# Kernel tuning notes

Measured on AMD Instinct MI355X. Metric: run time of the kernel, lower is better.

The kernel has to match this reference:

```python
import jax, jax.numpy as jnp
import numpy as np
import math

NUM_HEADS = 12


def setup_inputs() -> dict:
    key = jax.random.key(0)
    ks = jax.random.split(key, 8)
    B, H, W, C = 8, 32, 32, 768
    dh = C // NUM_HEADS
    s = 0.02
    return {
        "x": jax.random.normal(ks[0], (B, H, W, C), dtype=jnp.float32),
        "w_qkv": jax.random.normal(ks[1], (C, 3 * C), dtype=jnp.float32) * s,
        "b_qkv": jnp.zeros((3 * C,), dtype=jnp.float32),
        "w_out": jax.random.normal(ks[2], (C, C), dtype=jnp.float32) * s,
        "b_out": jnp.zeros((C,), dtype=jnp.float32),
        "rel_pos_h": jax.random.normal(ks[3], (2 * H - 1, dh), dtype=jnp.float32) * s,
        "rel_pos_w": jax.random.normal(ks[4], (2 * W - 1, dh), dtype=jnp.float32) * s,
    }


def reference(x, w_qkv, b_qkv, w_out, b_out, rel_pos_h, rel_pos_w):
    B, H, W, C = x.shape
    nh = NUM_HEADS
    dh = C // nh
    scale = math.sqrt(dh)

    # QKV projection: (B, H*W, 3C) -> (3, B*nh, H*W, dh)
    qkv = jnp.einsum("bhwc,cf->bhwf", x, w_qkv) + b_qkv
    qkv = qkv.reshape(B, H * W, 3, nh, dh).transpose(2, 0, 3, 1, 4)
    qkv = qkv.reshape(3, B * nh, H * W, dh)
    q, k, v = qkv[0], qkv[1], qkv[2]

    scores = jnp.einsum("bqd,bkd->bqk", q, k) / scale  # (B*nh, HW, HW)

    # Decomposed relative position bias (q_size == k_size == input_size,
    # so get_rel_pos is a pure gather, no interpolation).
    coords_h = jnp.arange(H)[:, None] - jnp.arange(H)[None, :] + (H - 1)
    coords_w = jnp.arange(W)[:, None] - jnp.arange(W)[None, :] + (W - 1)
    Rh = rel_pos_h[coords_h]  # (H, H, dh)
    Rw = rel_pos_w[coords_w]  # (W, W, dh)
    r_q = q.reshape(B * nh, H, W, dh)
    rel_h = jnp.einsum("bhwc,hkc->bhwk", r_q, Rh)  # (B*nh, H, W, H)
    rel_w = jnp.einsum("bhwc,wkc->bhwk", r_q, Rw)  # (B*nh, H, W, W)
    scores = (
        scores.reshape(B * nh, H, W, H, W)
        + rel_h[:, :, :, :, None]
        + rel_w[:, :, :, None, :]
    ).reshape(B * nh, H * W, H * W)

    weights = jax.nn.softmax(scores, axis=-1)
    out = jnp.einsum("bqk,bkd->bqd", weights, v)  # (B*nh, HW, dh)
    out = out.reshape(B, nh, H, W, dh).transpose(0, 2, 3, 1, 4).reshape(B, H, W, C)
    return jnp.einsum("bhwc,cf->bhwf", out, w_out) + b_out
```

## Files before the change

kernel.cpp:

```cpp
#include <hip/hip_runtime.h>
#include <stdint.h>

#define NH 12
#define DH 64
#define HW_ 32
#define SEQ 1024
#define CDIM 768
#define BATCH 8
#define BHN (BATCH*NH)

#define LOG2E 1.44269504f
#define KSCALE 0.18033688f

typedef unsigned short u16;
typedef __attribute__((ext_vector_type(4))) float f32x4;
typedef __attribute__((ext_vector_type(8))) short bf16x8;

static __device__ __forceinline__ u16 f2bf(float f) {
  union { float f; unsigned u; } v; v.f = f;
  unsigned r = v.u + 0x7fff + ((v.u >> 16) & 1);
  return (u16)(r >> 16);
}
static __device__ __forceinline__ float bf2f(u16 h) {
  union { unsigned u; float f; } v; v.u = ((unsigned)h) << 16;
  return v.f;
}
static __device__ __forceinline__ unsigned pk_bf2(float a, float b) {
  union { float f; unsigned u; } ua, ub; ua.f = a; ub.f = b;
  return __builtin_amdgcn_perm(ub.u + 0x8000u, ua.u + 0x8000u, 0x07060302u);
}

#define GLDS(gp, lp) __builtin_amdgcn_global_load_lds( \
  (const __attribute__((address_space(1))) unsigned int*)(gp), \
  (__attribute__((address_space(3))) unsigned int*)(lp), 16, 0, 0)

__global__ void k_cvt_x(const float* __restrict__ x, u16* __restrict__ xb, int n4) {
  int i = blockIdx.x * 256 + threadIdx.x;
  if (i < n4) {
    const float4 v = *(const float4*)(x + (size_t)i * 4);
    uint2 o;
    o.x = (unsigned)f2bf(v.x) | ((unsigned)f2bf(v.y) << 16);
    o.y = (unsigned)f2bf(v.z) | ((unsigned)f2bf(v.w) << 16);
    *(uint2*)(xb + (size_t)i * 4) = o;
  }
}

__global__ void k_transcvt(const float* __restrict__ w, u16* __restrict__ wt, int R, int C) {
  __shared__ float t[64][65];
  int c0 = blockIdx.x * 64, r0 = blockIdx.y * 64;
  #pragma unroll
  for (int i = 0; i < 16; ++i) {
    int r = threadIdx.y + i * 4;
    t[r][threadIdx.x] = w[(size_t)(r0 + r) * C + c0 + threadIdx.x];
  }
  __syncthreads();
  #pragma unroll
  for (int i = 0; i < 16; ++i) {
    int c = threadIdx.y + i * 4;
    wt[(size_t)(c0 + c) * R + r0 + threadIdx.x] = f2bf(t[threadIdx.x][c]);
  }
}

__global__ __launch_bounds__(256) void k_relbias2(
    const u16* __restrict__ Q, const float* __restrict__ rph,
    const float* __restrict__ rpw,
    float* __restrict__ bH, float* __restrict__ bW) {
  __shared__ float Gs[4][64][66];
  const int bh = blockIdx.y;
  const int tid = threadIdx.x, w = tid >> 6, l = tid & 63;
  const int rr = l & 15, g4 = l >> 4;
  const int p0 = blockIdx.x * 256 + w * 64;
  const u16* Qb = Q + ((size_t)bh * SEQ + p0) * DH;

  bf16x8 qa[4][2];
  #pragma unroll
  for (int rt = 0; rt < 4; ++rt)
    #pragma unroll
    for (int kk = 0; kk < 2; ++kk)
      qa[rt][kk] = *(const bf16x8*)&Qb[(size_t)(rt * 16 + rr) * DH + kk * 32 + g4 * 8];

  const int hq0 = p0 >> 5;
  #pragma unroll
  for (int g = 0; g < 2; ++g) {
    int hq = hq0 + g;
    #pragma unroll
    for (int ct = 0; ct < 2; ++ct) {
      bf16x8 bfr[2];
      #pragma unroll
      for (int kk = 0; kk < 2; ++kk) {
        const float* src = &rph[(size_t)(hq - (ct * 16 + rr) + 31) * DH + kk * 32 + g4 * 8];
        #pragma unroll
        for (int e = 0; e < 8; ++e) bfr[kk][e] = (short)f2bf(src[e]);
      }
      #pragma unroll
      for (int mt = 0; mt < 2; ++mt) {
        f32x4 acc = {};
        #pragma unroll
        for (int kk = 0; kk < 2; ++kk)
          acc = __builtin_amdgcn_mfma_f32_16x16x32_bf16(qa[g * 2 + mt][kk], bfr[kk], acc, 0, 0, 0);
        #pragma unroll
        for (int j = 0; j < 4; ++j) {
          int row = p0 + g * 32 + mt * 16 + g4 * 4 + j;
          bH[((size_t)bh * SEQ + row) * 32 + ct * 16 + rr] = acc[j] * LOG2E;
        }
      }
    }
  }

  #pragma unroll
  for (int jt = 0; jt < 4; ++jt) {
    int j_ = jt * 16 + rr; if (j_ > 62) j_ = 62;
    bf16x8 bfr[2];
    #pragma unroll
    for (int kk = 0; kk < 2; ++kk) {
      const float* src = &rpw[(size_t)j_ * DH + kk * 32 + g4 * 8];
      #pragma unroll
      for (int e = 0; e < 8; ++e) bfr[kk][e] = (short)f2bf(src[e]);
    }
    #pragma unroll
    for (int rt = 0; rt < 4; ++rt) {
      f32x4 acc = {};
      #pragma unroll
      for (int kk = 0; kk < 2; ++kk)
        acc = __builtin_amdgcn_mfma_f32_16x16x32_bf16(qa[rt][kk], bfr[kk], acc, 0, 0, 0);
      #pragma unroll
      for (int j = 0; j < 4; ++j)
        Gs[w][rt * 16 + g4 * 4 + j][jt * 16 + rr] = acc[j] * LOG2E;
    }
  }
  __syncthreads();
  #pragma unroll
  for (int wk = 0; wk < 32; ++wk)
    bW[((size_t)bh * SEQ + p0 + l) * 32 + wk] = Gs[w][l][(l & 31) - wk + 31];
}

template<int EPI, int NT>
__global__ __launch_bounds__(256) void k_gemm(
    const u16* __restrict__ A, const u16* __restrict__ Bt,
    const float* __restrict__ bias,
    void* __restrict__ o0, void* __restrict__ o1, void* __restrict__ o2,
    int nwg) {
  __shared__ u16 As[2][128][32];
  __shared__ u16 Bs[2][128][32];
  const int cpx = nwg >> 3;
  const int swz = (blockIdx.x & 7) * cpx + (blockIdx.x >> 3);
  const int tid = threadIdx.x, w = tid >> 6, l = tid & 63;
  const int wr = w >> 1, wc = w & 1;
  const int rr = l & 15, g4 = l >> 4;
  const int m0 = (swz / NT) * 128, n0 = (swz % NT) * 128;
  const int K = CDIM;
  f32x4 acc[4][4] = {};

  auto stage = [&](int buf, int t) {
    int k0 = t * 32;
    #pragma unroll
    for (int i = 0; i < 2; ++i) {
      int c = tid + i * 256;
      int row = c >> 2, kc = (c & 3) * 8;
      GLDS(A + (size_t)(m0 + row) * K + k0 + kc, ((u16*)As) + buf * 4096 + c * 8);
      GLDS(Bt + (size_t)(n0 + row) * K + k0 + kc, ((u16*)Bs) + buf * 4096 + c * 8);
    }
  };
  stage(0, 0);
  __syncthreads();
  for (int t = 0; t < K / 32; ++t) {
    const int cur = t & 1;
    if (t + 1 < K / 32) stage(cur ^ 1, t + 1);
    bf16x8 af[4], bfr[4];
    #pragma unroll
    for (int mm = 0; mm < 4; ++mm)
      af[mm] = *(const bf16x8*)(((const u16*)As) + cur * 4096 + (wr * 64 + mm * 16 + rr) * 32 + g4 * 8);
    #pragma unroll
    for (int nn = 0; nn < 4; ++nn)
      bfr[nn] = *(const bf16x8*)(((const u16*)Bs) + cur * 4096 + (wc * 64 + nn * 16 + rr) * 32 + g4 * 8);
    __builtin_amdgcn_s_setprio(1);
    #pragma unroll
    for (int mm = 0; mm < 4; ++mm)
      #pragma unroll
      for (int nn = 0; nn < 4; ++nn)
        acc[mm][nn] = __builtin_amdgcn_mfma_f32_16x16x32_bf16(af[mm], bfr[nn], acc[mm][nn], 0, 0, 0);
    __builtin_amdgcn_s_setprio(0);
    __syncthreads();
  }
  #pragma unroll
  for (int mm = 0; mm < 4; ++mm)
    #pragma unroll
    for (int nn = 0; nn < 4; ++nn) {
      int row0 = m0 + wr * 64 + mm * 16 + g4 * 4;
      int col = n0 + wc * 64 + nn * 16 + rr;
      float bb = bias[col];
      if (EPI == 0) {
        int which = col / CDIM, rem = col % CDIM;
        int hh = rem >> 6, d = rem & 63;
        int b = row0 >> 10, p = row0 & 1023;
        if (which == 2) {
          uint2 pk;
          pk.x = (unsigned)f2bf(acc[mm][nn][0] + bb) | ((unsigned)f2bf(acc[mm][nn][1] + bb) << 16);
          pk.y = (unsigned)f2bf(acc[mm][nn][2] + bb) | ((unsigned)f2bf(acc[mm][nn][3] + bb) << 16);
          *(uint2*)&((u16*)o2)[((size_t)(b * NH + hh) * DH + d) * SEQ + p] = pk;
        } else if (which == 1) {
          #pragma unroll
          for (int j = 0; j < 4; ++j)
            ((u16*)o1)[(((size_t)(b * NH + hh)) * SEQ + p + j) * DH + d] = f2bf((acc[mm][nn][j] + bb) * KSCALE);
        } else {
          #pragma unroll
          for (int j = 0; j < 4; ++j)
            ((u16*)o0)[(((size_t)(b * NH + hh)) * SEQ + p + j) * DH + d] = f2bf(acc[mm][nn][j] + bb);
        }
      } else {
        #pragma unroll
        for (int j = 0; j < 4; ++j)
          ((float*)o0)[(size_t)(row0 + j) * CDIM + col] = acc[mm][nn][j] + bb;
      }
    }
}

__global__ __launch_bounds__(256) void k_attn(
    const u16* __restrict__ Q, const u16* __restrict__ Kg,
    const u16* __restrict__ Vtg,
    const float* __restrict__ bHg, const float* __restrict__ bWg,
    u16* __restrict__ O) {
  __shared__ u16 Ks[2][64][64];
  __shared__ u16 Vs[2][64][64];
  __shared__ u16 Ps[4][32][72];
  const int bid = blockIdx.x;
  const int bhi = bid % 96;
  const int q0 = (bid / 96) * 128;
  const int tid = threadIdx.x, w = tid >> 6, l = tid & 63;
  const int rr = l & 15, g4 = l >> 4;
  const u16* Qb = Q + (size_t)bhi * SEQ * DH;
  const u16* Kb = Kg + (size_t)bhi * SEQ * DH;
  const u16* Vb = Vtg + (size_t)bhi * SEQ * DH;

  bf16x8 qf[2][2];
  #pragma unroll
  for (int mm = 0; mm < 2; ++mm)
    #pragma unroll
    for (int kk = 0; kk < 2; ++kk)
      qf[mm][kk] = *(const bf16x8*)&Qb[(size_t)(q0 + w * 32 + mm * 16 + rr) * DH + kk * 32 + g4 * 8];

  int ibase[2][4];
  float4 bwv[2][4];
  #pragma unroll
  for (int mm = 0; mm < 2; ++mm)
    #pragma unroll
    for (int j = 0; j < 4; ++j) {
      int p_e = q0 + w * 32 + mm * 16 + g4 * 4 + j;
      ibase[mm][j] = (bhi * SEQ + p_e) * 32;
      bwv[mm][j] = *(const float4*)&bWg[ibase[mm][j] + ((4 * rr) & 31)];
    }
  float lsum[2][4] = {};
  f32x4 oacc[2][4] = {};

  auto stageKV = [&](int buf, int t) {
    int k0 = t * 64;
    #pragma unroll
    for (int i = 0; i < 2; ++i) {
      int c = tid + i * 256;
      int row = c >> 3, ci = c & 7;
      int swk = ci ^ ((row >> 2) & 7);
      int swv = ci ^ (row & 7);
      GLDS(Kb + (size_t)(k0 + row) * DH + swk * 8, ((u16*)Ks) + buf * 4096 + c * 8);
      GLDS(Vb + (size_t)row * SEQ + k0 + swv * 8, ((u16*)Vs) + buf * 4096 + c * 8);
    }
  };
  stageKV(0, 0);
  __syncthreads();

  for (int t = 0; t < 16; ++t) {
    const int cur = t & 1;
    if (t + 1 < 16) stageKV(cur ^ 1, t + 1);

    bf16x8 kf[4][2];
    #pragma unroll
    for (int nn = 0; nn < 4; ++nn)
      #pragma unroll
      for (int kk = 0; kk < 2; ++kk) {
        int row = 4 * rr + nn;
        int ch = (kk * 4 + g4) ^ ((row >> 2) & 7);
        kf[nn][kk] = *(const bf16x8*)(((const u16*)Ks) + cur * 4096 + row * 64 + ch * 8);
      }
    f32x4 sc[2][4] = {};
    __builtin_amdgcn_s_setprio(1);
    #pragma unroll
    for (int mm = 0; mm < 2; ++mm)
      #pragma unroll
      for (int nn = 0; nn < 4; ++nn)
        #pragma unroll
        for (int kk = 0; kk < 2; ++kk)
          sc[mm][nn] = __builtin_amdgcn_mfma_f32_16x16x32_bf16(qf[mm][kk], kf[nn][kk], sc[mm][nn], 0, 0, 0);
    __builtin_amdgcn_s_setprio(0);

    #pragma unroll
    for (int mm = 0; mm < 2; ++mm)
      #pragma unroll
      for (int j = 0; j < 4; ++j) {
        float bh = bHg[ibase[mm][j] + t * 2 + (rr >> 3)];
        float v0 = __builtin_amdgcn_exp2f(sc[mm][0][j] + (bh + bwv[mm][j].x));
        float v1 = __builtin_amdgcn_exp2f(sc[mm][1][j] + (bh + bwv[mm][j].y));
        float v2 = __builtin_amdgcn_exp2f(sc[mm][2][j] + (bh + bwv[mm][j].z));
        float v3 = __builtin_amdgcn_exp2f(sc[mm][3][j] + (bh + bwv[mm][j].w));
        lsum[mm][j] += (v0 + v1) + (v2 + v3);
        uint2 pk;
        pk.x = pk_bf2(v0, v1);
        pk.y = pk_bf2(v2, v3);
        int prow = mm * 16 + g4 * 4 + j;
        *(uint2*)&Ps[w][prow][4 * rr] = pk;
      }

    bf16x8 pa[2][2], vf[4][2];
    #pragma unroll
    for (int mm = 0; mm < 2; ++mm)
      #pragma unroll
      for (int kk = 0; kk < 2; ++kk)
        pa[mm][kk] = *(const bf16x8*)&Ps[w][mm * 16 + rr][kk * 32 + g4 * 8];
    #pragma unroll
    for (int nn = 0; nn < 4; ++nn)
      #pragma unroll
      for (int kk = 0; kk < 2; ++kk) {
        int row = nn * 16 + rr;
        int ch = (kk * 4 + g4) ^ (row & 7);
        vf[nn][kk] = *(const bf16x8*)(((const u16*)Vs) + cur * 4096 + row * 64 + ch * 8);
      }
    __builtin_amdgcn_s_setprio(1);
    #pragma unroll
    for (int mm = 0; mm < 2; ++mm)
      #pragma unroll
      for (int nn = 0; nn < 4; ++nn)
        #pragma unroll
        for (int kk = 0; kk < 2; ++kk)
          oacc[mm][nn] = __builtin_amdgcn_mfma_f32_16x16x32_bf16(pa[mm][kk], vf[nn][kk], oacc[mm][nn], 0, 0, 0);
    __builtin_amdgcn_s_setprio(0);
    __syncthreads();
  }

  const int b = bhi / NH, h = bhi % NH;
  #pragma unroll
  for (int mm = 0; mm < 2; ++mm)
    #pragma unroll
    for (int j = 0; j < 4; ++j) {
      float lv = lsum[mm][j];
      #pragma unroll
      for (int off = 1; off < 16; off <<= 1) lv += __shfl_xor(lv, off);
      float inv = 1.0f / lv;
      int p = q0 + w * 32 + mm * 16 + g4 * 4 + j;
      #pragma unroll
      for (int nn = 0; nn < 4; ++nn) {
        int d = nn * 16 + rr;
        O[((size_t)(b * SEQ + p)) * CDIM + h * DH + d] = f2bf(oacc[mm][nn][j] * inv);
      }
    }
}

extern "C" void kernel_launch(void* const* d_in, const int* in_sizes, int n_in,
                              void* d_out, int out_size, void* d_ws, size_t ws_size,
                              hipStream_t stream) {
  const float* x     = (const float*)d_in[0];
  const float* w_qkv = (const float*)d_in[1];
  const float* b_qkv = (const float*)d_in[2];
  const float* w_out = (const float*)d_in[3];
  const float* b_out = (const float*)d_in[4];
  const float* rph   = (const float*)d_in[5];
  const float* rpw   = (const float*)d_in[6];
  float* out = (float*)d_out;
  char* ws = (char*)d_ws;

  const size_t SZ = (size_t)BHN * SEQ * DH * 2;
  u16* Xb    = (u16*)(ws);
  u16* Wqkvt = (u16*)(ws + SZ);
  u16* Woutt = (u16*)(ws + SZ + 3538944);
  u16* Qd    = (u16*)(ws + SZ + 4718592);
  u16* Kd    = (u16*)(ws + 2 * SZ + 4718592);
  u16* Vd    = (u16*)(ws + 3 * SZ + 4718592);
  u16* Vt    = (u16*)(ws + 4 * SZ + 4718592);
  float* bW  = (float*)(ws + 5 * SZ + 4718592);
  float* bH  = (float*)Vd;
  u16* Ob    = Xb;
  if (ws_size < 6 * SZ + 4718592) return;

  k_cvt_x<<<6144, 256, 0, stream>>>(x, Xb, 8192 * 768 / 4);
  k_transcvt<<<dim3(36, 12), dim3(64, 4), 0, stream>>>(w_qkv, Wqkvt, 768, 2304);
  k_transcvt<<<dim3(12, 12), dim3(64, 4), 0, stream>>>(w_out, Woutt, 768, 768);
  k_gemm<0, 18><<<1152, 256, 0, stream>>>(Xb, Wqkvt, b_qkv, Qd, Kd, Vt, 1152);
  k_relbias2<<<dim3(4, 96), 256, 0, stream>>>(Qd, rph, rpw, bH, bW);
  k_attn<<<768, 256, 0, stream>>>(Qd, Kd, Vt, bH, bW, Ob);
  k_gemm<1, 6><<<384, 256, 0, stream>>>(Ob, Woutt, b_out, out, nullptr, nullptr, 384);
}
```

Measured before the change: 163.4 us.

## Split attention block across 8 waves of 16 query rows each

The attention kernel now launches 512 threads per block, so each wave owns 16 query rows instead of 32. This halves per-thread accumulator and fragment registers and doubles the waves sharing each staged K/V tile; each thread now issues one async load per tile instead of two. The per-tile height bias global load is replaced by preloading 32 bias values into two registers per row and fetching the needed one with a cross-lane shuffle. The trade-off is that each wave re-reads the full K/V fragments from LDS for half as much MFMA work, raising LDS traffic per FLOP, and the block barrier now spans more waves.

New measurement: 156.3 us. 1.04x faster.

```diff
diff --git a/kernel.cpp b/kernel.cpp
--- a/kernel.cpp
+++ b/kernel.cpp
@@ -215,14 +215,14 @@
     }
 }
 
-__global__ __launch_bounds__(256) void k_attn(
+__global__ __launch_bounds__(512, 4) void k_attn(
     const u16* __restrict__ Q, const u16* __restrict__ Kg,
     const u16* __restrict__ Vtg,
     const float* __restrict__ bHg, const float* __restrict__ bWg,
     u16* __restrict__ O) {
   __shared__ u16 Ks[2][64][64];
   __shared__ u16 Vs[2][64][64];
-  __shared__ u16 Ps[4][32][72];
+  __shared__ u16 Ps[8][16][72];
   const int bid = blockIdx.x;
   const int bhi = bid % 96;
   const int q0 = (bid / 96) * 128;
@@ -232,37 +232,33 @@
   const u16* Kb = Kg + (size_t)bhi * SEQ * DH;
   const u16* Vb = Vtg + (size_t)bhi * SEQ * DH;
 
-  bf16x8 qf[2][2];
-  #pragma unroll
-  for (int mm = 0; mm < 2; ++mm)
-    #pragma unroll
-    for (int kk = 0; kk < 2; ++kk)
-      qf[mm][kk] = *(const bf16x8*)&Qb[(size_t)(q0 + w * 32 + mm * 16 + rr) * DH + kk * 32 + g4 * 8];
-
-  int ibase[2][4];
-  float4 bwv[2][4];
-  #pragma unroll
-  for (int mm = 0; mm < 2; ++mm)
-    #pragma unroll
-    for (int j = 0; j < 4; ++j) {
-      int p_e = q0 + w * 32 + mm * 16 + g4 * 4 + j;
-      ibase[mm][j] = (bhi * SEQ + p_e) * 32;
-      bwv[mm][j] = *(const float4*)&bWg[ibase[mm][j] + ((4 * rr) & 31)];
-    }
-  float lsum[2][4] = {};
-  f32x4 oacc[2][4] = {};
+  bf16x8 qf[2];
+  #pragma unroll
+  for (int kk = 0; kk < 2; ++kk)
+    qf[kk] = *(const bf16x8*)&Qb[(size_t)(q0 + w * 16 + rr) * DH + kk * 32 + g4 * 8];
+
+  float4 bwv[4];
+  float bh0[4], bh1[4];
+  float lsum[4] = {};
+  f32x4 oacc[4] = {};
+  #pragma unroll
+  for (int j = 0; j < 4; ++j) {
+    int p_e = q0 + w * 16 + g4 * 4 + j;
+    const float* bHrow = &bHg[((size_t)bhi * SEQ + p_e) * 32];
+    const float* bWrow = &bWg[((size_t)bhi * SEQ + p_e) * 32];
+    bwv[j] = *(const float4*)&bWrow[(4 * rr) & 31];
+    bh0[j] = bHrow[rr];
+    bh1[j] = bHrow[16 + rr];
+  }
 
   auto stageKV = [&](int buf, int t) {
     int k0 = t * 64;
-    #pragma unroll
-    for (int i = 0; i < 2; ++i) {
-      int c = tid + i * 256;
-      int row = c >> 3, ci = c & 7;
-      int swk = ci ^ ((row >> 2) & 7);
-      int swv = ci ^ (row & 7);
-      GLDS(Kb + (size_t)(k0 + row) * DH + swk * 8, ((u16*)Ks) + buf * 4096 + c * 8);
-      GLDS(Vb + (size_t)row * SEQ + k0 + swv * 8, ((u16*)Vs) + buf * 4096 + c * 8);
-    }
+    int c = tid;
+    int row = c >> 3, ci = c & 7;
+    int swk = ci ^ ((row >> 2) & 7);
+    int swv = ci ^ (row & 7);
+    GLDS(Kb + (size_t)(k0 + row) * DH + swk * 8, ((u16*)Ks) + buf * 4096 + c * 8);
+    GLDS(Vb + (size_t)row * SEQ + k0 + swv * 8, ((u16*)Vs) + buf * 4096 + c * 8);
   };
   stageKV(0, 0);
   __syncthreads();
@@ -280,40 +276,35 @@
         int ch = (kk * 4 + g4) ^ ((row >> 2) & 7);
         kf[nn][kk] = *(const bf16x8*)(((const u16*)Ks) + cur * 4096 + row * 64 + ch * 8);
       }
-    f32x4 sc[2][4] = {};
+    f32x4 sc[4] = {};
     __builtin_amdgcn_s_setprio(1);
     #pragma unroll
-    for (int mm = 0; mm < 2; ++mm)
-      #pragma unroll
-      for (int nn = 0; nn < 4; ++nn)
-        #pragma unroll
-        for (int kk = 0; kk < 2; ++kk)
-          sc[mm][nn] = __builtin_amdgcn_mfma_f32_16x16x32_bf16(qf[mm][kk], kf[nn][kk], sc[mm][nn], 0, 0, 0);
+    for (int nn = 0; nn < 4; ++nn)
+      #pragma unroll
+      for (int kk = 0; kk < 2; ++kk)
+        sc[nn] = __builtin_amdgcn_mfma_f32_16x16x32_bf16(qf[kk], kf[nn][kk], sc[nn], 0, 0, 0);
     __builtin_amdgcn_s_setprio(0);
 
-    #pragma unroll
-    for (int mm = 0; mm < 2; ++mm)
-      #pragma unroll
-      for (int j = 0; j < 4; ++j) {
-        float bh = bHg[ibase[mm][j] + t * 2 + (rr >> 3)];
-        float v0 = __builtin_amdgcn_exp2f(sc[mm][0][j] + (bh + bwv[mm][j].x));
-        float v1 = __builtin_amdgcn_exp2f(sc[mm][1][j] + (bh + bwv[mm][j].y));
-        float v2 = __builtin_amdgcn_exp2f(sc[mm][2][j] + (bh + bwv[mm][j].z));
-        float v3 = __builtin_amdgcn_exp2f(sc[mm][3][j] + (bh + bwv[mm][j].w));
-        lsum[mm][j] += (v0 + v1) + (v2 + v3);
-        uint2 pk;
-        pk.x = pk_bf2(v0, v1);
-        pk.y = pk_bf2(v2, v3);
-        int prow = mm * 16 + g4 * 4 + j;
-        *(uint2*)&Ps[w][prow][4 * rr] = pk;
-      }
-
-    bf16x8 pa[2][2], vf[4][2];
-    #pragma unroll
-    for (int mm = 0; mm < 2; ++mm)
-      #pragma unroll
-      for (int kk = 0; kk < 2; ++kk)
-        pa[mm][kk] = *(const bf16x8*)&Ps[w][mm * 16 + rr][kk * 32 + g4 * 8];
+    int srcl = (l & 48) | ((2 * t + (rr >> 3)) & 15);
+    #pragma unroll
+    for (int j = 0; j < 4; ++j) {
+      float bhsel = (t < 8) ? bh0[j] : bh1[j];
+      float bh = __shfl(bhsel, srcl);
+      float v0 = __builtin_amdgcn_exp2f(sc[0][j] + (bh + bwv[j].x));
+      float v1 = __builtin_amdgcn_exp2f(sc[1][j] + (bh + bwv[j].y));
+      float v2 = __builtin_amdgcn_exp2f(sc[2][j] + (bh + bwv[j].z));
+      float v3 = __builtin_amdgcn_exp2f(sc[3][j] + (bh + bwv[j].w));
+      lsum[j] += (v0 + v1) + (v2 + v3);
+      uint2 pk;
+      pk.x = pk_bf2(v0, v1);
+      pk.y = pk_bf2(v2, v3);
+      *(uint2*)&Ps[w][g4 * 4 + j][4 * rr] = pk;
+    }
+
+    bf16x8 pa[2], vf[4][2];
+    #pragma unroll
+    for (int kk = 0; kk < 2; ++kk)
+      pa[kk] = *(const bf16x8*)&Ps[w][rr][kk * 32 + g4 * 8];
     #pragma unroll
     for (int nn = 0; nn < 4; ++nn)
       #pragma unroll
@@ -324,32 +315,28 @@
       }
     __builtin_amdgcn_s_setprio(1);
     #pragma unroll
-    for (int mm = 0; mm < 2; ++mm)
-      #pragma unroll
-      for (int nn = 0; nn < 4; ++nn)
-        #pragma unroll
-        for (int kk = 0; kk < 2; ++kk)
-          oacc[mm][nn] = __builtin_amdgcn_mfma_f32_16x16x32_bf16(pa[mm][kk], vf[nn][kk], oacc[mm][nn], 0, 0, 0);
+    for (int nn = 0; nn < 4; ++nn)
+      #pragma unroll
+      for (int kk = 0; kk < 2; ++kk)
+        oacc[nn] = __builtin_amdgcn_mfma_f32_16x16x32_bf16(pa[kk], vf[nn][kk], oacc[nn], 0, 0, 0);
     __builtin_amdgcn_s_setprio(0);
     __syncthreads();
   }
 
   const int b = bhi / NH, h = bhi % NH;
   #pragma unroll
-  for (int mm = 0; mm < 2; ++mm)
-    #pragma unroll
-    for (int j = 0; j < 4; ++j) {
-      float lv = lsum[mm][j];
-      #pragma unroll
-      for (int off = 1; off < 16; off <<= 1) lv += __shfl_xor(lv, off);
-      float inv = 1.0f / lv;
-      int p = q0 + w * 32 + mm * 16 + g4 * 4 + j;
-      #pragma unroll
-      for (int nn = 0; nn < 4; ++nn) {
-        int d = nn * 16 + rr;
-        O[((size_t)(b * SEQ + p)) * CDIM + h * DH + d] = f2bf(oacc[mm][nn][j] * inv);
-      }
-    }
+  for (int j = 0; j < 4; ++j) {
+    float lv = lsum[j];
+    #pragma unroll
+    for (int off = 1; off < 16; off <<= 1) lv += __shfl_xor(lv, off);
+    float inv = 1.0f / lv;
+    int p = q0 + w * 16 + g4 * 4 + j;
+    #pragma unroll
+    for (int nn = 0; nn < 4; ++nn) {
+      int d = nn * 16 + rr;
+      O[((size_t)(b * SEQ + p)) * CDIM + h * DH + d] = f2bf(oacc[nn][j] * inv);
+    }
+  }
 }
 
 extern "C" void kernel_launch(void* const* d_in, const int* in_sizes, int n_in,
@@ -383,6 +370,6 @@
   k_transcvt<<<dim3(12, 12), dim3(64, 4), 0, stream>>>(w_out, Woutt, 768, 768);
   k_gemm<0, 18><<<1152, 256, 0, stream>>>(Xb, Wqkvt, b_qkv, Qd, Kd, Vt, 1152);
   k_relbias2<<<dim3(4, 96), 256, 0, stream>>>(Qd, rph, rpw, bH, bW);
-  k_attn<<<768, 256, 0, stream>>>(Qd, Kd, Vt, bH, bW, Ob);
+  k_attn<<<768, 512, 0, stream>>>(Qd, Kd, Vt, bH, bW, Ob);
   k_gemm<1, 6><<<384, 256, 0, stream>>>(Ob, Woutt, b_out, out, nullptr, nullptr, 384);
 }
```
